# Performance work log

Measured on AMD Instinct MI355X. Metric: run time of the kernel, lower is better.

Reference implementation:

```python
import jax, jax.numpy as jnp
import numpy as np

KERNEL_NUM = 21
SIGMA = 0.1
EXACT_SIGMA = 0.001

def _kernel_params(k=KERNEL_NUM, sigma=SIGMA, exact_sigma=EXACT_SIGMA):
    step = 1.0 / (k - 1)
    left = -1.0 + step
    right = 1.0 - step
    mu = np.hstack([np.arange(left, right, (right - left) / (k - 2)), right, 1.0])
    sig = np.where(mu == 1.0, exact_sigma, sigma)
    return jnp.asarray(mu, jnp.float32), jnp.asarray(sig, jnp.float32)

MU, SIG = _kernel_params()

def setup_inputs() -> dict:
    key = jax.random.key(0)
    ks = jax.random.split(key, 11)
    B, LQ, LD, V, E = 1024, 20, 200, 100000, 128
    return {
        "q1": jax.random.randint(ks[0], (B, LQ), 0, V),
        "d1": jax.random.randint(ks[1], (B, LD), 0, V),
        "q2": jax.random.randint(ks[2], (B, LQ), 0, V),
        "d2": jax.random.randint(ks[3], (B, LD), 0, V),
        "emb": jax.random.normal(ks[4], (V, E), jnp.float32),
        "W1": jax.random.normal(ks[5], (10, 21), jnp.float32) * 0.1,
        "b1": jax.random.normal(ks[6], (10,), jnp.float32) * 0.1,
        "W2": jax.random.normal(ks[7], (5, 10), jnp.float32) * 0.1,
        "b2": jax.random.normal(ks[8], (5,), jnp.float32) * 0.1,
        "W3": jax.random.normal(ks[9], (1, 5), jnp.float32) * 0.1,
        "b3": jax.random.normal(ks[10], (1,), jnp.float32) * 0.1,
    }

def _matching_matrix(emb, q_ids, d_ids, alpha=1e-6):
    q = emb[q_ids]  # [B,LQ,E]
    d = emb[d_ids]  # [B,LD,E]
    nom = jnp.einsum('bqe,bde->bqd', q, d)
    qn = jnp.sqrt(jnp.sum(q * q, axis=2) + alpha)  # [B,LQ]
    dn = jnp.sqrt(jnp.sum(d * d, axis=2) + alpha)  # [B,LD]
    return nom / (qn[:, :, None] * dn[:, None, :])  # [B,LQ,LD]

def _apply_kernels(M):
    # M: [B,LQ,LD] -> phi: [B,LQ,LD,K]
    phi = jnp.exp(-jnp.square(M[..., None] - MU) / (2.0 * SIG * SIG))
    return jnp.sum(jnp.log1p(jnp.sum(phi, axis=2)), axis=1)  # [B,K]

def _mlp(x, W1, b1, W2, b2, W3, b3):
    x = jax.nn.relu(x)
    x = x @ W1.T + b1
    x = jax.nn.relu(x)
    x = x @ W2.T + b2
    x = jax.nn.relu(x)
    return x @ W3.T + b3  # [B,1]

def _predict(emb, q, d, W1, b1, W2, b2, W3, b3):
    M = _matching_matrix(emb, q, d)
    k = _apply_kernels(M)
    return _mlp(k, W1, b1, W2, b2, W3, b3)

def reference(q1, d1, q2, d2, emb, W1, b1, W2, b2, W3, b3):
    l1 = _predict(emb, q1, d1, W1, b1, W2, b2, W3, b3)
    l2 = _predict(emb, q2, d2, W1, b1, W2, b2, W3, b3)
    return jax.nn.sigmoid(l1 - l2)  # [B,1]
```

## Files before the change

### kernel.cpp

```cpp
#include <hip/hip_runtime.h>
#include <hip/hip_bf16.h>

#define NB 1024
#define LQ 20
#define LD 200
#define E4 32
#define NK 21
#define NTILE 13

typedef __attribute__((ext_vector_type(8))) short bf16x8;
typedef __attribute__((ext_vector_type(4))) float f32x4;

__device__ __forceinline__ unsigned cvt2(float lo, float hi) {
    __hip_bfloat162 h = __float22bfloat162_rn(make_float2(lo, hi));
    unsigned u;
    __builtin_memcpy(&u, &h, 4);
    return u;
}
__device__ __forceinline__ float lo2f(unsigned p) { return __builtin_bit_cast(float, p << 16); }
__device__ __forceinline__ float hi2f(unsigned p) { return __builtin_bit_cast(float, p & 0xFFFF0000u); }

__device__ __forceinline__ bf16x8 make_frag(float4 f0, float4 f1, float& sq) {
    union { unsigned u[4]; bf16x8 v; } r;
    r.u[0] = cvt2(f0.x, f0.y);
    r.u[1] = cvt2(f0.z, f0.w);
    r.u[2] = cvt2(f1.x, f1.y);
    r.u[3] = cvt2(f1.z, f1.w);
    #pragma unroll
    for (int i = 0; i < 4; ++i) {
        const float a = lo2f(r.u[i]); sq = fmaf(a, a, sq);
        const float b = hi2f(r.u[i]); sq = fmaf(b, b, sq);
    }
    return r.v;
}

__device__ __forceinline__ float fast_exp2(float x) {
#if __has_builtin(__builtin_amdgcn_exp2f)
    return __builtin_amdgcn_exp2f(x);
#else
    return __expf(x * 0.69314718056f);
#endif
}

__device__ __forceinline__ void rbf_accum(float m, float* S) {
    const float x = m - 0.05f;
    const float p = fast_exp2(-72.13475204f * x * x);
    S[10] += p;
    float u = fast_exp2(fmaf(m, 14.4269504089f, -1.44269504089f));
    float q = p;
    #pragma unroll
    for (int k = 11; k <= 19; ++k) {
        q *= u;
        S[k] += q;
        u *= 0.36787944117f;
    }
    float v = fast_exp2(m * -14.4269504089f);
    q = p;
    #pragma unroll
    for (int k = 9; k >= 0; --k) {
        q *= v;
        S[k] += q;
        v *= 0.36787944117f;
    }
    const float d = m - 1.0f;
    S[20] += fast_exp2(-721347.5204f * d * d);
}

__global__ __launch_bounds__(256, 2) void knrm_main(
    const int* __restrict__ q1, const int* __restrict__ d1,
    const int* __restrict__ q2, const int* __restrict__ d2,
    const float* __restrict__ emb,
    const float* __restrict__ W1, const float* __restrict__ b1,
    const float* __restrict__ W2, const float* __restrict__ b2,
    const float* __restrict__ W3, const float* __restrict__ b3,
    float* __restrict__ out)
{
    __shared__ float sPhiW[4][LQ][NK];
    __shared__ float sX[2][NK];
    __shared__ float sH1[2][10];
    __shared__ float sH2[2][5];

    const int b    = blockIdx.x;
    const int t    = threadIdx.x;
    const int lane = t & 63, wave = t >> 6;
    const int pred = wave >> 1, wv = wave & 1;
    const int c    = lane & 15, quad = lane >> 4;
    const int* __restrict__ qi = pred ? q2 : q1;
    const int* __restrict__ di = pred ? d2 : d1;
    const float4* emb4 = (const float4*)emb;

    int qid[2];
    #pragma unroll
    for (int Mt = 0; Mt < 2; ++Mt) {
        int row = Mt * 16 + c; row = row < LQ ? row : LQ - 1;
        qid[Mt] = qi[b * LQ + row];
    }
    int idv[7];
    #pragma unroll
    for (int tt = 0; tt < 7; ++tt) {
        const int tile = wv + 2 * tt;
        int j = tile * 16 + c; j = j < LD ? j : LD - 1;
        idv[tt] = (tile < NTILE) ? di[b * LD + j] : 0;
    }

    bf16x8 aF[2][4];
    float rqA = 0.f, rqB = 0.f;
    #pragma unroll
    for (int Mt = 0; Mt < 2; ++Mt) {
        const float4* qb = emb4 + (size_t)(unsigned)qid[Mt] * E4;
        float qs = 0.f;
        #pragma unroll
        for (int ks = 0; ks < 4; ++ks) {
            float4 f0 = qb[ks * 8 + quad * 2];
            float4 f1 = qb[ks * 8 + quad * 2 + 1];
            aF[Mt][ks] = make_frag(f0, f1, qs);
        }
        if (Mt == 1 && c >= LQ - 16) {
            #pragma unroll
            for (int ks = 0; ks < 4; ++ks) aF[Mt][ks] = (bf16x8)0;
            qs = 0.f;
        }
        qs += __shfl_xor(qs, 16);
        qs += __shfl_xor(qs, 32);
        const float rq = rsqrtf(qs + 1e-6f);
        if (Mt == 0) rqA = rq; else rqB = rq;
    }

    float S0[NK], S1[NK];
    #pragma unroll
    for (int k = 0; k < NK; ++k) { S0[k] = 0.f; S1[k] = 0.f; }

    #pragma unroll
    for (int tt = 0; tt < 7; ++tt) {
        const int tile = wv + 2 * tt;
        if (tile >= NTILE) break;

        const float4* db = emb4 + (size_t)(unsigned)idv[tt] * E4;
        bf16x8 bF[4];
        float dsq = 0.f;
        #pragma unroll
        for (int ks = 0; ks < 4; ++ks) {
            float4 f0 = db[ks * 8 + quad * 2];
            float4 f1 = db[ks * 8 + quad * 2 + 1];
            bF[ks] = make_frag(f0, f1, dsq);
        }
        if (tile * 16 + c >= LD) {
            #pragma unroll
            for (int ks = 0; ks < 4; ++ks) bF[ks] = (bf16x8)0;
            dsq = 0.f;
        }
        dsq += __shfl_xor(dsq, 16);
        dsq += __shfl_xor(dsq, 32);
        const float rdc = rsqrtf(dsq + 1e-6f);
        float rdv[4];
        #pragma unroll
        for (int r = 0; r < 4; ++r) rdv[r] = __shfl(rdc, quad * 4 + r);

        f32x4 acc0 = {0.f, 0.f, 0.f, 0.f};
        f32x4 acc1 = {0.f, 0.f, 0.f, 0.f};
        #pragma unroll
        for (int ks = 0; ks < 4; ++ks) {
            acc0 = __builtin_amdgcn_mfma_f32_16x16x32_bf16(bF[ks], aF[0][ks], acc0, 0, 0, 0);
            acc1 = __builtin_amdgcn_mfma_f32_16x16x32_bf16(bF[ks], aF[1][ks], acc1, 0, 0, 0);
        }

        #pragma unroll
        for (int r = 0; r < 4; ++r)
            rbf_accum(acc0[r] * rdv[r] * rqA, S0);

        float m1[4];
        #pragma unroll
        for (int r = 0; r < 4; ++r) m1[r] = acc1[r] * rdv[r] * rqB;
        const int src = (lane & 48) | ((lane >> 2) & 3);
        const float g0 = __shfl(m1[0], src);
        const float g1 = __shfl(m1[1], src);
        const float g2 = __shfl(m1[2], src);
        const float g3 = __shfl(m1[3], src);
        const int rsel = lane & 3;
        const float mv = (rsel == 0) ? g0 : (rsel == 1) ? g1 : (rsel == 2) ? g2 : g3;
        rbf_accum(mv, S1);
    }

    #pragma unroll
    for (int k = 0; k < NK; ++k) {
        S0[k] += __shfl_xor(S0[k], 16);
        S0[k] += __shfl_xor(S0[k], 32);
        S1[k] += __shfl_xor(S1[k], 1);
        S1[k] += __shfl_xor(S1[k], 2);
        S1[k] += __shfl_xor(S1[k], 16);
        S1[k] += __shfl_xor(S1[k], 32);
    }
    if (quad == 0) {
        #pragma unroll
        for (int k = 0; k < NK; ++k) sPhiW[wave][c][k] = S0[k];
    }
    if ((lane & 51) == 0) {
        #pragma unroll
        for (int k = 0; k < NK; ++k) sPhiW[wave][16 + (lane >> 2)][k] = S1[k];
    }
    __syncthreads();

    const int ew = t >> 6, et = t & 63;

    if (ew < 2 && et < NK) {
        const float mu_t = 0.1f * (float)et - 0.95f;
        const float pad  = (et < 20) ? 8.0f * fast_exp2(-72.13475204f * mu_t * mu_t) : 0.0f;
        float s = 0.f;
        #pragma unroll
        for (int i = 0; i < LQ; ++i) {
            const float v = sPhiW[2 * ew][i][et] + sPhiW[2 * ew + 1][i][et] - pad;
            s += __logf(1.0f + v);
        }
        sX[ew][et] = fmaxf(s, 0.f);
    }
    __syncthreads();

    if (ew < 2 && et < 10) {
        float v = b1[et];
        #pragma unroll
        for (int k = 0; k < NK; ++k) v += W1[et * NK + k] * sX[ew][k];
        sH1[ew][et] = fmaxf(v, 0.f);
    }
    __syncthreads();

    if (ew < 2 && et < 5) {
        float v = b2[et];
        #pragma unroll
        for (int k = 0; k < 10; ++k) v += W2[et * 10 + k] * sH1[ew][k];
        sH2[ew][et] = fmaxf(v, 0.f);
    }
    __syncthreads();

    if (t == 0) {
        float l0 = b3[0], l1 = b3[0];
        #pragma unroll
        for (int k = 0; k < 5; ++k) {
            l0 += W3[k] * sH2[0][k];
            l1 += W3[k] * sH2[1][k];
        }
        out[b] = 1.0f / (1.0f + __expf(l1 - l0));
    }
}

extern "C" void kernel_launch(void* const* d_in, const int* in_sizes, int n_in,
                              void* d_out, int out_size, void* d_ws, size_t ws_size,
                              hipStream_t stream) {
    knrm_main<<<NB, 256, 0, stream>>>(
        (const int*)d_in[0], (const int*)d_in[1],
        (const int*)d_in[2], (const int*)d_in[3],
        (const float*)d_in[4],
        (const float*)d_in[5], (const float*)d_in[6],
        (const float*)d_in[7], (const float*)d_in[8],
        (const float*)d_in[9], (const float*)d_in[10],
        (float*)d_out);
}
```

Before: 148.7 us.

## Software-pipeline doc embedding loads across tiles and compute norms in fp32

Replaces the fully unrolled tile loop with a rolled loop that prefetches the next tile's document embedding row (and the index two tiles ahead) while the current tile's MFMA and RBF work runs. This hides gather latency behind compute. Norms are now computed from the fp32 values instead of the rounded bf16 values, which removes the unpack ops but changes numerics slightly. The rolled loop drops some unrolling benefits and keeps eight float4 prefetch registers live.

```diff
diff --git a/kernel.cpp b/kernel.cpp
--- a/kernel.cpp
+++ b/kernel.cpp
@@ -17,21 +17,22 @@
     __builtin_memcpy(&u, &h, 4);
     return u;
 }
-__device__ __forceinline__ float lo2f(unsigned p) { return __builtin_bit_cast(float, p << 16); }
-__device__ __forceinline__ float hi2f(unsigned p) { return __builtin_bit_cast(float, p & 0xFFFF0000u); }
-
-__device__ __forceinline__ bf16x8 make_frag(float4 f0, float4 f1, float& sq) {
+
+__device__ __forceinline__ bf16x8 pack8(float4 f0, float4 f1) {
     union { unsigned u[4]; bf16x8 v; } r;
     r.u[0] = cvt2(f0.x, f0.y);
     r.u[1] = cvt2(f0.z, f0.w);
     r.u[2] = cvt2(f1.x, f1.y);
     r.u[3] = cvt2(f1.z, f1.w);
-    #pragma unroll
-    for (int i = 0; i < 4; ++i) {
-        const float a = lo2f(r.u[i]); sq = fmaf(a, a, sq);
-        const float b = hi2f(r.u[i]); sq = fmaf(b, b, sq);
-    }
     return r.v;
+}
+
+__device__ __forceinline__ float sq8(float4 f0, float4 f1, float s) {
+    s = fmaf(f0.x, f0.x, s); s = fmaf(f0.y, f0.y, s);
+    s = fmaf(f0.z, f0.z, s); s = fmaf(f0.w, f0.w, s);
+    s = fmaf(f1.x, f1.x, s); s = fmaf(f1.y, f1.y, s);
+    s = fmaf(f1.z, f1.z, s); s = fmaf(f1.w, f1.w, s);
+    return s;
 }
 
 __device__ __forceinline__ float fast_exp2(float x) {
@@ -89,80 +90,112 @@
     const int* __restrict__ di = pred ? d2 : d1;
     const float4* emb4 = (const float4*)emb;
 
-    int qid[2];
-    #pragma unroll
-    for (int Mt = 0; Mt < 2; ++Mt) {
-        int row = Mt * 16 + c; row = row < LQ ? row : LQ - 1;
-        qid[Mt] = qi[b * LQ + row];
-    }
-    int idv[7];
-    #pragma unroll
-    for (int tt = 0; tt < 7; ++tt) {
-        const int tile = wv + 2 * tt;
-        int j = tile * 16 + c; j = j < LD ? j : LD - 1;
-        idv[tt] = (tile < NTILE) ? di[b * LD + j] : 0;
+    const int qid0 = qi[b * LQ + c];
+    const int r1   = 16 + c;
+    const int qid1 = qi[b * LQ + (r1 < LQ ? r1 : LQ - 1)];
+    int tile = wv;
+    const int j0 = tile * 16 + c;
+    const int id0 = di[b * LD + (j0 < LD ? j0 : LD - 1)];
+    int idn;
+    {
+        const int jn = j0 + 32;
+        idn = di[b * LD + (jn < LD ? jn : LD - 1)];
+    }
+
+    float4 ld0, ld1, ld2, ld3, ld4, ld5, ld6, ld7;
+    {
+        const float4* db = emb4 + (size_t)(unsigned)id0 * E4;
+        ld0 = db[quad * 2];      ld1 = db[quad * 2 + 1];
+        ld2 = db[8 + quad * 2];  ld3 = db[8 + quad * 2 + 1];
+        ld4 = db[16 + quad * 2]; ld5 = db[16 + quad * 2 + 1];
+        ld6 = db[24 + quad * 2]; ld7 = db[24 + quad * 2 + 1];
     }
 
     bf16x8 aF[2][4];
-    float rqA = 0.f, rqB = 0.f;
-    #pragma unroll
-    for (int Mt = 0; Mt < 2; ++Mt) {
-        const float4* qb = emb4 + (size_t)(unsigned)qid[Mt] * E4;
-        float qs = 0.f;
+    float rqA, rqB;
+    {
+        const float4* qb0 = emb4 + (size_t)(unsigned)qid0 * E4;
+        const float4* qb1 = emb4 + (size_t)(unsigned)qid1 * E4;
+        float qs0 = 0.f, qs1 = 0.f;
         #pragma unroll
         for (int ks = 0; ks < 4; ++ks) {
-            float4 f0 = qb[ks * 8 + quad * 2];
-            float4 f1 = qb[ks * 8 + quad * 2 + 1];
-            aF[Mt][ks] = make_frag(f0, f1, qs);
-        }
-        if (Mt == 1 && c >= LQ - 16) {
+            float4 f0 = qb0[ks * 8 + quad * 2];
+            float4 f1 = qb0[ks * 8 + quad * 2 + 1];
+            qs0 = sq8(f0, f1, qs0);
+            aF[0][ks] = pack8(f0, f1);
+            float4 g0 = qb1[ks * 8 + quad * 2];
+            float4 g1 = qb1[ks * 8 + quad * 2 + 1];
+            qs1 = sq8(g0, g1, qs1);
+            aF[1][ks] = pack8(g0, g1);
+        }
+        if (c >= LQ - 16) {
             #pragma unroll
-            for (int ks = 0; ks < 4; ++ks) aF[Mt][ks] = (bf16x8)0;
-            qs = 0.f;
-        }
-        qs += __shfl_xor(qs, 16);
-        qs += __shfl_xor(qs, 32);
-        const float rq = rsqrtf(qs + 1e-6f);
-        if (Mt == 0) rqA = rq; else rqB = rq;
+            for (int ks = 0; ks < 4; ++ks) aF[1][ks] = (bf16x8)0;
+            qs1 = 0.f;
+        }
+        qs0 += __shfl_xor(qs0, 16); qs0 += __shfl_xor(qs0, 32);
+        qs1 += __shfl_xor(qs1, 16); qs1 += __shfl_xor(qs1, 32);
+        rqA = rsqrtf(qs0 + 1e-6f);
+        rqB = rsqrtf(qs1 + 1e-6f);
     }
 
     float S0[NK], S1[NK];
     #pragma unroll
     for (int k = 0; k < NK; ++k) { S0[k] = 0.f; S1[k] = 0.f; }
 
-    #pragma unroll
-    for (int tt = 0; tt < 7; ++tt) {
-        const int tile = wv + 2 * tt;
-        if (tile >= NTILE) break;
-
-        const float4* db = emb4 + (size_t)(unsigned)idv[tt] * E4;
-        bf16x8 bF[4];
+    #pragma unroll 1
+    while (true) {
+        if (tile == NTILE - 1 && c >= (LD - (NTILE - 1) * 16)) {
+            ld0 = ld1 = ld2 = ld3 = ld4 = ld5 = ld6 = ld7 = make_float4(0.f, 0.f, 0.f, 0.f);
+        }
+
         float dsq = 0.f;
-        #pragma unroll
-        for (int ks = 0; ks < 4; ++ks) {
-            float4 f0 = db[ks * 8 + quad * 2];
-            float4 f1 = db[ks * 8 + quad * 2 + 1];
-            bF[ks] = make_frag(f0, f1, dsq);
-        }
-        if (tile * 16 + c >= LD) {
-            #pragma unroll
-            for (int ks = 0; ks < 4; ++ks) bF[ks] = (bf16x8)0;
-            dsq = 0.f;
-        }
+        f32x4 acc0 = {0.f, 0.f, 0.f, 0.f};
+        f32x4 acc1 = {0.f, 0.f, 0.f, 0.f};
+        {
+            dsq = sq8(ld0, ld1, dsq);
+            bf16x8 bFk = pack8(ld0, ld1);
+            acc0 = __builtin_amdgcn_mfma_f32_16x16x32_bf16(bFk, aF[0][0], acc0, 0, 0, 0);
+            acc1 = __builtin_amdgcn_mfma_f32_16x16x32_bf16(bFk, aF[1][0], acc1, 0, 0, 0);
+        }
+        {
+            dsq = sq8(ld2, ld3, dsq);
+            bf16x8 bFk = pack8(ld2, ld3);
+            acc0 = __builtin_amdgcn_mfma_f32_16x16x32_bf16(bFk, aF[0][1], acc0, 0, 0, 0);
+            acc1 = __builtin_amdgcn_mfma_f32_16x16x32_bf16(bFk, aF[1][1], acc1, 0, 0, 0);
+        }
+        {
+            dsq = sq8(ld4, ld5, dsq);
+            bf16x8 bFk = pack8(ld4, ld5);
+            acc0 = __builtin_amdgcn_mfma_f32_16x16x32_bf16(bFk, aF[0][2], acc0, 0, 0, 0);
+            acc1 = __builtin_amdgcn_mfma_f32_16x16x32_bf16(bFk, aF[1][2], acc1, 0, 0, 0);
+        }
+        {
+            dsq = sq8(ld6, ld7, dsq);
+            bf16x8 bFk = pack8(ld6, ld7);
+            acc0 = __builtin_amdgcn_mfma_f32_16x16x32_bf16(bFk, aF[0][3], acc0, 0, 0, 0);
+            acc1 = __builtin_amdgcn_mfma_f32_16x16x32_bf16(bFk, aF[1][3], acc1, 0, 0, 0);
+        }
+
+        const int ntile = tile + 2;
+        if (ntile < NTILE) {
+            const float4* db = emb4 + (size_t)(unsigned)idn * E4;
+            ld0 = db[quad * 2];      ld1 = db[quad * 2 + 1];
+            ld2 = db[8 + quad * 2];  ld3 = db[8 + quad * 2 + 1];
+            ld4 = db[16 + quad * 2]; ld5 = db[16 + quad * 2 + 1];
+            ld6 = db[24 + quad * 2]; ld7 = db[24 + quad * 2 + 1];
+            if (ntile + 2 < NTILE) {
+                const int jn2 = (ntile + 2) * 16 + c;
+                idn = di[b * LD + (jn2 < LD ? jn2 : LD - 1)];
+            }
+        }
+
         dsq += __shfl_xor(dsq, 16);
         dsq += __shfl_xor(dsq, 32);
         const float rdc = rsqrtf(dsq + 1e-6f);
         float rdv[4];
         #pragma unroll
         for (int r = 0; r < 4; ++r) rdv[r] = __shfl(rdc, quad * 4 + r);
-
-        f32x4 acc0 = {0.f, 0.f, 0.f, 0.f};
-        f32x4 acc1 = {0.f, 0.f, 0.f, 0.f};
-        #pragma unroll
-        for (int ks = 0; ks < 4; ++ks) {
-            acc0 = __builtin_amdgcn_mfma_f32_16x16x32_bf16(bF[ks], aF[0][ks], acc0, 0, 0, 0);
-            acc1 = __builtin_amdgcn_mfma_f32_16x16x32_bf16(bF[ks], aF[1][ks], acc1, 0, 0, 0);
-        }
 
         #pragma unroll
         for (int r = 0; r < 4; ++r)
@@ -179,6 +212,9 @@
         const int rsel = lane & 3;
         const float mv = (rsel == 0) ? g0 : (rsel == 1) ? g1 : (rsel == 2) ? g2 : g3;
         rbf_accum(mv, S1);
+
+        tile += 2;
+        if (tile >= NTILE) break;
     }
 
     #pragma unroll
```

Result: faster. 137.7 us (-7.4%).
